# Performance work log

Hardware: AMD Instinct MI355X
Metric: run time of the kernel (lower is better)

The kernel has to match this reference:

```python
import jax, jax.numpy as jnp
import numpy as np

N_QUBITS = 12
N_LAYERS = 2
PATCH = 16
NPS = 14  # patches per side for 224/16
N_PATCHES = NPS * NPS
SCALE = 1.0 / np.sqrt(N_QUBITS)


def _butterfly_gates(n):
    # Faithful replication of QuantumOrthogonalLayer.butterfly_circuit indexing:
    # param_idx increments even when the (idx1, idx2) pair is skipped.
    gates, pidx = [], 0
    n_bl = int(np.ceil(np.log2(n)))
    for layer in range(n_bl):
        stride = 2 ** layer
        for start in range(0, n - stride, 2 * stride):
            for off in range(stride):
                i1, i2 = start + off, start + off + stride
                if i1 < n and i2 < n:
                    gates.append((pidx, i1, i2))
                pidx += 1
    nppl = sum(2 ** (n_bl - 1 - i) * 2 ** i for i in range(n_bl))  # n_params() = 32
    return gates, nppl

GATES, NPPL = _butterfly_gates(N_QUBITS)

# Pauli-Z sign table: qubit 0 is the most-significant bit of the flattened state index.
_bits = (np.arange(2 ** N_QUBITS)[:, None] >> np.arange(N_QUBITS - 1, -1, -1)[None, :]) & 1
Z_SIGNS = jnp.asarray(1.0 - 2.0 * _bits, dtype=jnp.float32)  # (4096, 12)


def _rbs_u(theta):
    # 4x4 real unitary of RY(2t,w1); CNOT(w1,w2); RY(-2t,w1); CNOT(w1,w2)
    c, s = jnp.cos(theta), jnp.sin(theta)
    c2, s2, cs = c * c, s * s, c * s
    return jnp.stack([
        jnp.stack([c2, s2, -cs, cs]),
        jnp.stack([s2, c2, cs, -cs]),
        jnp.stack([cs, -cs, c2, s2]),
        jnp.stack([-cs, cs, s2, c2]),
    ])


def _apply_2q(state, U, i, j):
    # state: (P, 2, 2, ..., 2); apply U to qubit axes i, j
    st = jnp.moveaxis(state, (1 + i, 1 + j), (-2, -1))
    shp = st.shape
    st = st.reshape(shp[:-2] + (4,)) @ U.T
    return jnp.moveaxis(st.reshape(shp), (-2, -1), (1 + i, 1 + j))


@jax.checkpoint
def quantum_expvals(features, params):
    # features: (P, n_qubits) angles; params: (N_LAYERS * NPPL,)
    P = features.shape[0]
    half = 0.5 * features
    amp = jnp.stack([jnp.cos(half), jnp.sin(half)], axis=-1)  # (P, n, 2) RY(x)|0>
    state = jnp.ones((P, 1), features.dtype)
    for q in range(N_QUBITS):  # product-state angle encoding
        state = (state[:, :, None] * amp[:, q][:, None, :]).reshape(P, -1)
    state = state.reshape((P,) + (2,) * N_QUBITS)
    for l in range(N_LAYERS):
        base = l * NPPL
        for pidx, w1, w2 in GATES:
            state = _apply_2q(state, _rbs_u(params[base + pidx]), w1, w2)
    probs = state.reshape(P, -1) ** 2
    return probs @ Z_SIGNS  # (P, n_qubits) <Z_i>


def setup_inputs() -> dict:
    key = jax.random.key(0)
    ks = jax.random.split(key, 6)
    x = jax.random.normal(ks[0], (4, 3, 224, 224), dtype=jnp.float32)
    W_proj = jax.random.normal(ks[1], (N_QUBITS, PATCH * PATCH), dtype=jnp.float32) / np.sqrt(PATCH * PATCH)
    b_proj = jnp.zeros((N_QUBITS,), jnp.float32)
    q_params = 0.1 * jax.random.normal(ks[2], (N_LAYERS * NPPL,), dtype=jnp.float32)
    k_params = 0.1 * jax.random.normal(ks[3], (N_LAYERS * NPPL,), dtype=jnp.float32)
    v_params = 0.1 * jax.random.normal(ks[4], (N_LAYERS * NPPL,), dtype=jnp.float32)
    W_cls = jax.random.normal(ks[5], (1000, N_PATCHES * N_QUBITS), dtype=jnp.float32) / np.sqrt(N_PATCHES * N_QUBITS)
    b_cls = jnp.zeros((1000,), jnp.float32)
    return {"x": x, "W_proj": W_proj, "b_proj": b_proj, "q_params": q_params,
            "k_params": k_params, "v_params": v_params, "W_cls": W_cls, "b_cls": b_cls}


def reference(x, W_proj, b_proj, q_params, k_params, v_params, W_cls, b_cls):
    B = x.shape[0]
    xg = jnp.mean(x, axis=1)  # channel average -> (B, H, W)
    patches = xg.reshape(B, NPS, PATCH, NPS, PATCH).transpose(0, 1, 3, 2, 4)
    patches = patches.reshape(B, N_PATCHES, PATCH * PATCH)
    proj = patches @ W_proj.T + b_proj  # (B, n_patches, n_qubits)
    feats = proj.reshape(-1, N_QUBITS)
    Q = quantum_expvals(feats, q_params).reshape(B, N_PATCHES, N_QUBITS)
    K = quantum_expvals(feats, k_params).reshape(B, N_PATCHES, N_QUBITS)
    V = quantum_expvals(feats, v_params).reshape(B, N_PATCHES, N_QUBITS)
    attn = jax.nn.softmax(jnp.einsum('bqd,bkd->bqk', Q, K) * SCALE, axis=-1)
    out = jnp.einsum('bqk,bkd->bqd', attn, V)  # (B, n_patches, n_qubits)
    logits = out.reshape(B, -1) @ W_cls.T + b_cls
    return logits
```

## Files before the change

kernel.cpp:

```cpp
#include <hip/hip_runtime.h>
#include <math.h>

#define NQ        12
#define NPS       14
#define NPATCH    196
#define NB        4
#define NCLS      1000
#define FEATDIM   2352
#define SCALE_F   0.28867513459481287f

constexpr int PRa[6][5] = {
    { 0, 1, 2, 3, 4},
    { 4, 5, 6, 7, 8},
    { 9,10,11, 0, 8},
    { 0, 4, 5, 8, 1},
    { 1, 6, 9,10, 2},
    { 7,10,11, 2, 3},
};
constexpr int PTa[6][7] = {
    {10, 5, 6, 7,11, 8, 9},
    { 1, 0, 3,10, 2,11, 9},
    { 2, 1, 4, 6, 7, 5, 3},
    { 7, 2, 6, 9,11,10, 3},
    { 0, 7, 4, 5, 8,11, 3},
    { 5, 0, 1, 6, 8, 4, 9},
};
constexpr int  IYa[6]  = {0, 4, 3, 0, 3, 3};
constexpr bool BARa[6] = {false, true, false, false, true, false};

constexpr int cwgt(int X, int q) {
    for (int k = 0; k < 4; ++k) if (PRa[X][k] == q) return 1 << k;
    for (int m = 0; m < 7; ++m) if (PTa[X][m] == q) return 17 << m;
    return 0;
}
constexpr int rimm3(int X, int Y, int IY, int rc) {
    int s = 0;
    for (int j = 0; j < 4; ++j)
        if ((rc >> j) & 1) s += cwgt(X, PRa[Y][j + (j >= IY ? 1 : 0)]);
    return s;
}
constexpr int expand(int rc, int IY) {
    return (rc & ((1 << IY) - 1)) | ((rc >> IY) << (IY + 1));
}

__device__ __forceinline__ void wait_lgkm() {
    __asm__ __volatile__("s_waitcnt lgkmcnt(0)" ::: "memory");
}

template<int TI>
__device__ __forceinline__ void relayout3(float amp[32], float* lds, int tid) {
    constexpr int X = TI, Y = (TI + 1) % 6, IY = IYa[TI];
    constexpr bool BAR = BARa[TI];
    float* w = lds + 17 * tid;
    #pragma unroll
    for (int rc = 0; rc < 16; ++rc) w[rc] = amp[rc];
    if (BAR) __syncthreads(); else wait_lgkm();
    int base = 0;
    #pragma unroll
    for (int j = 0; j < 7; ++j)
        base += ((tid >> j) & 1) ? cwgt(X, PTa[Y][j]) : 0;
    float tmp[16];
    #pragma unroll
    for (int rc = 0; rc < 16; ++rc)
        tmp[rc] = lds[base + rimm3(X, Y, IY, rc)];
    if (BAR) __syncthreads(); else wait_lgkm();
    #pragma unroll
    for (int rc = 0; rc < 16; ++rc) w[rc] = amp[16 + rc];
    if (BAR) __syncthreads(); else wait_lgkm();
    #pragma unroll
    for (int rc = 0; rc < 16; ++rc)
        amp[expand(rc, IY) | (1 << IY)] = lds[base + rimm3(X, Y, IY, rc)];
    if (BAR) __syncthreads();
    #pragma unroll
    for (int rc = 0; rc < 16; ++rc) amp[expand(rc, IY)] = tmp[rc];
}

template<int MI, int MJ>
__device__ __forceinline__ void apply_gate(float amp[32], float gc, float gs) {
    #pragma unroll
    for (int m = 0; m < 32; ++m) {
        if (m & (MI | MJ)) continue;
        float a0 = amp[m], a1 = amp[m | MJ], a2 = amp[m | MI], a3 = amp[m | MI | MJ];
        float p  = a0 + a1, q  = a0 - a1;
        float p2 = a2 + a3, q2 = a2 - a3;
        float t1 = 0.5f * p  + gc * q  - gs * q2;
        float t2 = 0.5f * p2 + gc * q2 + gs * q;
        amp[m]           = t1;
        amp[m | MJ]      = p  - t1;
        amp[m | MI]      = t2;
        amp[m | MI | MJ] = p2 - t2;
    }
}

template<int CTRL>
__device__ __forceinline__ float dppadd(float x) {
    int s = __builtin_amdgcn_update_dpp(0, __float_as_int(x), CTRL, 0xf, 0xf, true);
    return x + __int_as_float(s);
}
__device__ __forceinline__ float wave_sum(float x) {
    x = dppadd<0x111>(x);
    x = dppadd<0x112>(x);
    x = dppadd<0x114>(x);
    x = dppadd<0x118>(x);
    x = dppadd<0x142>(x);
    x = dppadd<0x143>(x);
    return x;
}

__global__ __launch_bounds__(128, 4) void qcirc_kernel(
    const float* __restrict__ x,
    const float* __restrict__ Wp,
    const float* __restrict__ bproj,
    const float* __restrict__ qp,
    const float* __restrict__ kp,
    const float* __restrict__ vp,
    float* __restrict__ qkv)
{
    __shared__ __align__(16) float lds[2176];
    __shared__ float chs[NQ], shs[NQ];
    __shared__ float gC[40], gS[40];
    __shared__ float red2[2][12];

    const int tid = threadIdx.x;
    const int p = blockIdx.x, b = blockIdx.y, c = blockIdx.z;
    const int bp = b * NPATCH + p;
    const float* params = (c == 0) ? qp : (c == 1) ? kp : vp;
    const int lane = tid & 63, wv = tid >> 6;

    float part[NQ];
    #pragma unroll
    for (int q = 0; q < NQ; ++q) part[q] = 0.0f;
    {
        int py = p / NPS, px = p % NPS;
        const float* xb = x + (size_t)b * 3 * 224 * 224;
        #pragma unroll
        for (int k = 0; k < 2; ++k) {
            int pix = tid + 128 * k;
            int off = (py * 16 + (pix >> 4)) * 224 + px * 16 + (pix & 15);
            float v = (xb[off] + xb[off + 50176] + xb[off + 100352]) * (1.0f / 3.0f);
            #pragma unroll
            for (int q = 0; q < NQ; ++q) part[q] += v * Wp[q * 256 + pix];
        }
    }
    if (tid < 40) {
        int l = tid / 20, g = tid - l * 20;
        float th = params[l * 32 + g];
        gC[tid] = 0.5f * cosf(2.0f * th);
        gS[tid] = 0.5f * sinf(2.0f * th);
    }
    #pragma unroll
    for (int q = 0; q < NQ; ++q) part[q] = wave_sum(part[q]);
    if (lane == 63) {
        #pragma unroll
        for (int q = 0; q < NQ; ++q) red2[wv][q] = part[q];
    }
    __syncthreads();
    if (tid < NQ) {
        float h = 0.5f * (red2[0][tid] + red2[1][tid] + bproj[tid]);
        chs[tid] = cosf(h); shs[tid] = sinf(h);
    }
    __syncthreads();

    float amp[32];
    {
        float hi = ((tid &  1) ? shs[10] : chs[10]) *
                   ((tid &  2) ? shs[5]  : chs[5])  *
                   ((tid &  4) ? shs[6]  : chs[6])  *
                   ((tid &  8) ? shs[7]  : chs[7])  *
                   ((tid & 16) ? shs[11] : chs[11]) *
                   ((tid & 32) ? shs[8]  : chs[8])  *
                   ((tid & 64) ? shs[9]  : chs[9]);
        float pA[8], pB[4];
        #pragma unroll
        for (int i = 0; i < 8; ++i)
            pA[i] = ((i & 1) ? shs[0] : chs[0]) * ((i & 2) ? shs[1] : chs[1]) *
                    ((i & 4) ? shs[2] : chs[2]);
        #pragma unroll
        for (int i = 0; i < 4; ++i)
            pB[i] = ((i & 1) ? shs[3] : chs[3]) * ((i & 2) ? shs[4] : chs[4]);
        #pragma unroll
        for (int r = 0; r < 32; ++r) amp[r] = pA[r & 7] * pB[r >> 3] * hi;
    }

    #pragma unroll 1
    for (int l = 0; l < 2; ++l) {
        const int bb = l * 20;
        apply_gate<1, 2>(amp, gC[bb+0], gS[bb+0]);
        apply_gate<4, 8>(amp, gC[bb+1], gS[bb+1]);
        apply_gate<1, 4>(amp, gC[bb+6], gS[bb+6]);
        apply_gate<2, 8>(amp, gC[bb+7], gS[bb+7]);
        relayout3<0>(amp, lds, tid);
        apply_gate<1, 2>(amp, gC[bb+2], gS[bb+2]);
        apply_gate<4, 8>(amp, gC[bb+3], gS[bb+3]);
        apply_gate<1, 4>(amp, gC[bb+8], gS[bb+8]);
        apply_gate<2, 8>(amp, gC[bb+9], gS[bb+9]);
        relayout3<1>(amp, lds, tid);
        apply_gate<16,1>(amp, gC[bb+4],  gS[bb+4]);
        apply_gate<2, 4>(amp, gC[bb+5],  gS[bb+5]);
        apply_gate<16,2>(amp, gC[bb+10], gS[bb+10]);
        apply_gate<1, 4>(amp, gC[bb+11], gS[bb+11]);
        relayout3<2>(amp, lds, tid);
        apply_gate<1, 2>(amp, gC[bb+12], gS[bb+12]);
        apply_gate<16,4>(amp, gC[bb+13], gS[bb+13]);
        apply_gate<1, 8>(amp, gC[bb+16], gS[bb+16]);
        relayout3<3>(amp, lds, tid);
        apply_gate<16,2>(amp, gC[bb+14], gS[bb+14]);
        apply_gate<1, 4>(amp, gC[bb+17], gS[bb+17]);
        relayout3<4>(amp, lds, tid);
        apply_gate<16,1>(amp, gC[bb+15], gS[bb+15]);
        apply_gate<8, 2>(amp, gC[bb+18], gS[bb+18]);
        apply_gate<16,4>(amp, gC[bb+19], gS[bb+19]);
        if (l == 0) relayout3<5>(amp, lds, tid);
    }

    float T, Sq7, Sq10, Sq11, Sq2, Sq3;
    {
        float t1[16]; Sq7 = 0.0f;
        #pragma unroll
        for (int i = 0; i < 16; ++i) {
            float e = amp[2*i] * amp[2*i], o = amp[2*i+1] * amp[2*i+1];
            t1[i] = e + o; Sq7 += e - o;
        }
        float t2[8]; Sq10 = 0.0f;
        #pragma unroll
        for (int i = 0; i < 8; ++i) { t2[i] = t1[2*i] + t1[2*i+1]; Sq10 += t1[2*i] - t1[2*i+1]; }
        float t3[4]; Sq11 = 0.0f;
        #pragma unroll
        for (int i = 0; i < 4; ++i) { t3[i] = t2[2*i] + t2[2*i+1]; Sq11 += t2[2*i] - t2[2*i+1]; }
        float t4[2]; Sq2 = 0.0f;
        #pragma unroll
        for (int i = 0; i < 2; ++i) { t4[i] = t3[2*i] + t3[2*i+1]; Sq2 += t3[2*i] - t3[2*i+1]; }
        T = t4[0] + t4[1]; Sq3 = t4[0] - t4[1];
    }
    float Vq5 = (tid &  1) ? -T : T;
    float Vq0 = (tid &  2) ? -T : T;
    float Vq1 = (tid &  4) ? -T : T;
    float Vq6 = (tid &  8) ? -T : T;
    float Vq8 = (tid & 16) ? -T : T;
    float Vq4 = (tid & 32) ? -T : T;
    T    = wave_sum(T);
    Vq5  = wave_sum(Vq5);  Vq0  = wave_sum(Vq0);  Vq1  = wave_sum(Vq1);
    Vq6  = wave_sum(Vq6);  Vq8  = wave_sum(Vq8);  Vq4  = wave_sum(Vq4);
    Sq7  = wave_sum(Sq7);  Sq10 = wave_sum(Sq10); Sq11 = wave_sum(Sq11);
    Sq2  = wave_sum(Sq2);  Sq3  = wave_sum(Sq3);
    if (lane == 63) {
        red2[wv][0]  = Vq0;  red2[wv][1]  = Vq1;  red2[wv][2]  = Sq2;
        red2[wv][3]  = Sq3;  red2[wv][4]  = Vq4;  red2[wv][5]  = Vq5;
        red2[wv][6]  = Vq6;  red2[wv][7]  = Sq7;  red2[wv][8]  = Vq8;
        red2[wv][9]  = T;    red2[wv][10] = Sq10; red2[wv][11] = Sq11;
    }
    __syncthreads();
    if (tid < NQ) {
        float v1 = red2[1][tid];
        float s = red2[0][tid] + ((tid == 9) ? -v1 : v1);
        qkv[((size_t)c * (NB * NPATCH) + bp) * NQ + tid] = s;
    }
}

__global__ __launch_bounds__(256) void attn_kernel(
    const float* __restrict__ qkv,
    float* __restrict__ outb)
{
    int tid = threadIdx.x;
    int qp = blockIdx.x, b = blockIdx.y;
    const float* Q = qkv;
    const float* K = qkv + NB * NPATCH * NQ;
    const float* V = qkv + 2 * NB * NPATCH * NQ;

    __shared__ float redm[4], reds[4], redv[4][NQ];

    float4 q0 = ((const float4*)(Q + (b * NPATCH + qp) * NQ))[0];
    float4 q1 = ((const float4*)(Q + (b * NPATCH + qp) * NQ))[1];
    float4 q2 = ((const float4*)(Q + (b * NPATCH + qp) * NQ))[2];

    float score = -1e30f;
    float4 v0, v1, v2;
    if (tid < NPATCH) {
        const float4* K4 = (const float4*)(K + (b * NPATCH + tid) * NQ);
        float4 k0 = K4[0], k1 = K4[1], k2 = K4[2];
        float s = q0.x*k0.x + q0.y*k0.y + q0.z*k0.z + q0.w*k0.w
                + q1.x*k1.x + q1.y*k1.y + q1.z*k1.z + q1.w*k1.w
                + q2.x*k2.x + q2.y*k2.y + q2.z*k2.z + q2.w*k2.w;
        score = s * SCALE_F;
        const float4* V4 = (const float4*)(V + (b * NPATCH + tid) * NQ);
        v0 = V4[0]; v1 = V4[1]; v2 = V4[2];
    }
    float m = score;
    #pragma unroll
    for (int o = 32; o > 0; o >>= 1) m = fmaxf(m, __shfl_down(m, o));
    int lane = tid & 63, wv = tid >> 6;
    if (lane == 0) redm[wv] = m;
    __syncthreads();
    float maxv = fmaxf(fmaxf(redm[0], redm[1]), fmaxf(redm[2], redm[3]));

    float w = (tid < NPATCH) ? expf(score - maxv) : 0.0f;
    float sm = w;
    #pragma unroll
    for (int o = 32; o > 0; o >>= 1) sm += __shfl_down(sm, o);
    if (lane == 0) reds[wv] = sm;

    float part[NQ];
    #pragma unroll
    for (int d = 0; d < NQ; d++) part[d] = 0.0f;
    if (tid < NPATCH) {
        part[0] = w*v0.x; part[1] = w*v0.y; part[2]  = w*v0.z; part[3]  = w*v0.w;
        part[4] = w*v1.x; part[5] = w*v1.y; part[6]  = w*v1.z; part[7]  = w*v1.w;
        part[8] = w*v2.x; part[9] = w*v2.y; part[10] = w*v2.z; part[11] = w*v2.w;
    }
    #pragma unroll
    for (int d = 0; d < NQ; d++) {
        #pragma unroll
        for (int o = 32; o > 0; o >>= 1) part[d] += __shfl_down(part[d], o);
    }
    if (lane == 0) {
        #pragma unroll
        for (int d = 0; d < NQ; d++) redv[wv][d] = part[d];
    }
    __syncthreads();
    if (tid < NQ) {
        float sumv = reds[0] + reds[1] + reds[2] + reds[3];
        float s = redv[0][tid] + redv[1][tid] + redv[2][tid] + redv[3][tid];
        outb[(size_t)b * FEATDIM + qp * NQ + tid] = s / sumv;
    }
}

__global__ __launch_bounds__(256) void cls_kernel(
    const float* __restrict__ outb,
    const float* __restrict__ Wc,
    const float* __restrict__ bc,
    float* __restrict__ logits)
{
    int o = blockIdx.x, tid = threadIdx.x;
    float acc[NB] = {0.0f, 0.0f, 0.0f, 0.0f};
    const float4* w4 = (const float4*)(Wc + (size_t)o * FEATDIM);
    for (int j = tid; j < FEATDIM / 4; j += 256) {
        float4 w = w4[j];
        #pragma unroll
        for (int b = 0; b < NB; b++) {
            float4 ov = ((const float4*)(outb + (size_t)b * FEATDIM))[j];
            acc[b] += w.x*ov.x + w.y*ov.y + w.z*ov.z + w.w*ov.w;
        }
    }
    #pragma unroll
    for (int b = 0; b < NB; b++) {
        #pragma unroll
        for (int off = 32; off > 0; off >>= 1) acc[b] += __shfl_down(acc[b], off);
    }
    __shared__ float red[4][NB];
    int lane = tid & 63, wv = tid >> 6;
    if (lane == 0) {
        #pragma unroll
        for (int b = 0; b < NB; b++) red[wv][b] = acc[b];
    }
    __syncthreads();
    if (tid < NB) {
        float s = red[0][tid] + red[1][tid] + red[2][tid] + red[3][tid];
        logits[(size_t)tid * NCLS + o] = s + bc[o];
    }
}

extern "C" void kernel_launch(void* const* d_in, const int* in_sizes, int n_in,
                              void* d_out, int out_size, void* d_ws, size_t ws_size,
                              hipStream_t stream) {
    const float* x     = (const float*)d_in[0];
    const float* Wp    = (const float*)d_in[1];
    const float* bproj = (const float*)d_in[2];
    const float* qp    = (const float*)d_in[3];
    const float* kp    = (const float*)d_in[4];
    const float* vp    = (const float*)d_in[5];
    const float* Wc    = (const float*)d_in[6];
    const float* bc    = (const float*)d_in[7];
    float* logits = (float*)d_out;

    float* ws   = (float*)d_ws;
    float* qkv  = ws;
    float* outb = ws + 28224;

    qcirc_kernel<<<dim3(NPATCH, NB, 3), 128, 0, stream>>>(x, Wp, bproj, qp, kp, vp, qkv);
    attn_kernel <<<dim3(NPATCH, NB),    256, 0, stream>>>(qkv, outb);
    cls_kernel  <<<NCLS,                256, 0, stream>>>(outb, Wc, bc, logits);
}
```

Before: 120.2 us.

## Redesign qubit-to-register mapping with float4 LDS relayouts swapping three qubits

Replaces the six scalar relayout stages, which each exchanged four qubits through LDS in two half passes, with eight relayout stages that keep qubits 2,3 permanently in registers and swap three qubits. Each stage now stores and loads 32 amplitudes as float4 vectors with a 36-float padded stride. The gate schedule, initial product-state ordering and final Pauli-Z reduction are remapped to match. The aim is fewer, wider LDS instructions and fewer waits per relayout, at the cost of more relayout stages and doubling LDS to 4608 floats, which may reduce occupancy.

```diff
diff --git a/kernel.cpp b/kernel.cpp
--- a/kernel.cpp
+++ b/kernel.cpp
@@ -9,38 +9,38 @@
 #define FEATDIM   2352
 #define SCALE_F   0.28867513459481287f
 
-constexpr int PRa[6][5] = {
-    { 0, 1, 2, 3, 4},
-    { 4, 5, 6, 7, 8},
-    { 9,10,11, 0, 8},
-    { 0, 4, 5, 8, 1},
-    { 1, 6, 9,10, 2},
-    { 7,10,11, 2, 3},
+constexpr int PRa[8][5] = {
+    {2,3,0,1, 4},
+    {2,3,4,5, 6},
+    {2,3,5,6, 7},
+    {2,3,0,4, 6},
+    {2,3,8,9,10},
+    {2,3,9,10,11},
+    {2,3,0,8,10},
+    {2,3,1,5, 9},
 };
-constexpr int PTa[6][7] = {
-    {10, 5, 6, 7,11, 8, 9},
-    { 1, 0, 3,10, 2,11, 9},
-    { 2, 1, 4, 6, 7, 5, 3},
-    { 7, 2, 6, 9,11,10, 3},
-    { 0, 7, 4, 5, 8,11, 3},
-    { 5, 0, 1, 6, 8, 4, 9},
+constexpr int PTa[8][7] = {
+    {5,6,7,8,9,10,11},
+    {7,0,1,8,9,10,11},
+    {0,1,4,8,9,10,11},
+    {8,9,10,1,5,7,11},
+    {4,0,1,5,6,7,11},
+    {0,1,8,5,6,7,4},
+    {1,5,9,6,7,11,4},
+    {6,0,11,7,8,10,4},
 };
-constexpr int  IYa[6]  = {0, 4, 3, 0, 3, 3};
-constexpr bool BARa[6] = {false, true, false, false, true, false};
+constexpr bool BARa[8] = {false,false,false,false,true,false,false,true};
 
 constexpr int cwgt(int X, int q) {
-    for (int k = 0; k < 4; ++k) if (PRa[X][k] == q) return 1 << k;
-    for (int m = 0; m < 7; ++m) if (PTa[X][m] == q) return 17 << m;
+    for (int k = 0; k < 5; ++k) if (PRa[X][k] == q) return 1 << k;
+    for (int m = 0; m < 7; ++m) if (PTa[X][m] == q) return 36 << m;
     return 0;
 }
-constexpr int rimm3(int X, int Y, int IY, int rc) {
+constexpr int rimmB(int X, int Y, int a) {
     int s = 0;
-    for (int j = 0; j < 4; ++j)
-        if ((rc >> j) & 1) s += cwgt(X, PRa[Y][j + (j >= IY ? 1 : 0)]);
+    for (int j = 0; j < 3; ++j)
+        if ((a >> j) & 1) s += cwgt(X, PRa[Y][2 + j]);
     return s;
-}
-constexpr int expand(int rc, int IY) {
-    return (rc & ((1 << IY) - 1)) | ((rc >> IY) << (IY + 1));
 }
 
 __device__ __forceinline__ void wait_lgkm() {
@@ -48,31 +48,23 @@
 }
 
 template<int TI>
-__device__ __forceinline__ void relayout3(float amp[32], float* lds, int tid) {
-    constexpr int X = TI, Y = (TI + 1) % 6, IY = IYa[TI];
-    constexpr bool BAR = BARa[TI];
-    float* w = lds + 17 * tid;
-    #pragma unroll
-    for (int rc = 0; rc < 16; ++rc) w[rc] = amp[rc];
-    if (BAR) __syncthreads(); else wait_lgkm();
+__device__ __forceinline__ void relayoutB(float amp[32], float* lds, int tid) {
+    constexpr int X = TI, Y = (TI + 1) & 7;
+    float4* dst = (float4*)(lds + 36 * tid);
+    #pragma unroll
+    for (int k = 0; k < 8; ++k)
+        dst[k] = make_float4(amp[4*k], amp[4*k+1], amp[4*k+2], amp[4*k+3]);
+    if (BARa[TI]) __syncthreads(); else wait_lgkm();
     int base = 0;
     #pragma unroll
     for (int j = 0; j < 7; ++j)
         base += ((tid >> j) & 1) ? cwgt(X, PTa[Y][j]) : 0;
-    float tmp[16];
-    #pragma unroll
-    for (int rc = 0; rc < 16; ++rc)
-        tmp[rc] = lds[base + rimm3(X, Y, IY, rc)];
-    if (BAR) __syncthreads(); else wait_lgkm();
-    #pragma unroll
-    for (int rc = 0; rc < 16; ++rc) w[rc] = amp[16 + rc];
-    if (BAR) __syncthreads(); else wait_lgkm();
-    #pragma unroll
-    for (int rc = 0; rc < 16; ++rc)
-        amp[expand(rc, IY) | (1 << IY)] = lds[base + rimm3(X, Y, IY, rc)];
-    if (BAR) __syncthreads();
-    #pragma unroll
-    for (int rc = 0; rc < 16; ++rc) amp[expand(rc, IY)] = tmp[rc];
+    #pragma unroll
+    for (int a = 0; a < 8; ++a) {
+        float4 v = *(const float4*)(lds + base + rimmB(X, Y, a));
+        amp[4*a+0] = v.x; amp[4*a+1] = v.y; amp[4*a+2] = v.z; amp[4*a+3] = v.w;
+    }
+    if (BARa[TI]) __syncthreads();
 }
 
 template<int MI, int MJ>
@@ -116,7 +108,7 @@
     const float* __restrict__ vp,
     float* __restrict__ qkv)
 {
-    __shared__ __align__(16) float lds[2176];
+    __shared__ __align__(16) float lds[4608];
     __shared__ float chs[NQ], shs[NQ];
     __shared__ float gC[40], gS[40];
     __shared__ float red2[2][12];
@@ -163,21 +155,21 @@
 
     float amp[32];
     {
-        float hi = ((tid &  1) ? shs[10] : chs[10]) *
-                   ((tid &  2) ? shs[5]  : chs[5])  *
-                   ((tid &  4) ? shs[6]  : chs[6])  *
-                   ((tid &  8) ? shs[7]  : chs[7])  *
-                   ((tid & 16) ? shs[11] : chs[11]) *
-                   ((tid & 32) ? shs[8]  : chs[8])  *
-                   ((tid & 64) ? shs[9]  : chs[9]);
+        float hi = ((tid &  1) ? shs[5]  : chs[5])  *
+                   ((tid &  2) ? shs[6]  : chs[6])  *
+                   ((tid &  4) ? shs[7]  : chs[7])  *
+                   ((tid &  8) ? shs[8]  : chs[8])  *
+                   ((tid & 16) ? shs[9]  : chs[9])  *
+                   ((tid & 32) ? shs[10] : chs[10]) *
+                   ((tid & 64) ? shs[11] : chs[11]);
         float pA[8], pB[4];
         #pragma unroll
         for (int i = 0; i < 8; ++i)
-            pA[i] = ((i & 1) ? shs[0] : chs[0]) * ((i & 2) ? shs[1] : chs[1]) *
-                    ((i & 4) ? shs[2] : chs[2]);
+            pA[i] = ((i & 1) ? shs[2] : chs[2]) * ((i & 2) ? shs[3] : chs[3]) *
+                    ((i & 4) ? shs[0] : chs[0]);
         #pragma unroll
         for (int i = 0; i < 4; ++i)
-            pB[i] = ((i & 1) ? shs[3] : chs[3]) * ((i & 2) ? shs[4] : chs[4]);
+            pB[i] = ((i & 1) ? shs[1] : chs[1]) * ((i & 2) ? shs[4] : chs[4]);
         #pragma unroll
         for (int r = 0; r < 32; ++r) amp[r] = pA[r & 7] * pB[r >> 3] * hi;
     }
@@ -185,74 +177,76 @@
     #pragma unroll 1
     for (int l = 0; l < 2; ++l) {
         const int bb = l * 20;
-        apply_gate<1, 2>(amp, gC[bb+0], gS[bb+0]);
-        apply_gate<4, 8>(amp, gC[bb+1], gS[bb+1]);
-        apply_gate<1, 4>(amp, gC[bb+6], gS[bb+6]);
-        apply_gate<2, 8>(amp, gC[bb+7], gS[bb+7]);
-        relayout3<0>(amp, lds, tid);
-        apply_gate<1, 2>(amp, gC[bb+2], gS[bb+2]);
-        apply_gate<4, 8>(amp, gC[bb+3], gS[bb+3]);
-        apply_gate<1, 4>(amp, gC[bb+8], gS[bb+8]);
-        apply_gate<2, 8>(amp, gC[bb+9], gS[bb+9]);
-        relayout3<1>(amp, lds, tid);
-        apply_gate<16,1>(amp, gC[bb+4],  gS[bb+4]);
-        apply_gate<2, 4>(amp, gC[bb+5],  gS[bb+5]);
-        apply_gate<16,2>(amp, gC[bb+10], gS[bb+10]);
-        apply_gate<1, 4>(amp, gC[bb+11], gS[bb+11]);
-        relayout3<2>(amp, lds, tid);
-        apply_gate<1, 2>(amp, gC[bb+12], gS[bb+12]);
-        apply_gate<16,4>(amp, gC[bb+13], gS[bb+13]);
-        apply_gate<1, 8>(amp, gC[bb+16], gS[bb+16]);
-        relayout3<3>(amp, lds, tid);
-        apply_gate<16,2>(amp, gC[bb+14], gS[bb+14]);
-        apply_gate<1, 4>(amp, gC[bb+17], gS[bb+17]);
-        relayout3<4>(amp, lds, tid);
-        apply_gate<16,1>(amp, gC[bb+15], gS[bb+15]);
-        apply_gate<8, 2>(amp, gC[bb+18], gS[bb+18]);
-        apply_gate<16,4>(amp, gC[bb+19], gS[bb+19]);
-        if (l == 0) relayout3<5>(amp, lds, tid);
-    }
-
-    float T, Sq7, Sq10, Sq11, Sq2, Sq3;
+        apply_gate<4, 8>(amp, gC[bb+0], gS[bb+0]);
+        apply_gate<1, 2>(amp, gC[bb+1], gS[bb+1]);
+        apply_gate<4, 1>(amp, gC[bb+6], gS[bb+6]);
+        apply_gate<8, 2>(amp, gC[bb+7], gS[bb+7]);
+        relayoutB<0>(amp, lds, tid);
+        apply_gate<4, 8>(amp, gC[bb+2], gS[bb+2]);
+        relayoutB<1>(amp, lds, tid);
+        apply_gate<8,16>(amp, gC[bb+3],  gS[bb+3]);
+        apply_gate<4,16>(amp, gC[bb+9],  gS[bb+9]);
+        apply_gate<2,16>(amp, gC[bb+15], gS[bb+15]);
+        relayoutB<2>(amp, lds, tid);
+        apply_gate<8,16>(amp, gC[bb+8],  gS[bb+8]);
+        apply_gate<4, 8>(amp, gC[bb+12], gS[bb+12]);
+        apply_gate<1,16>(amp, gC[bb+14], gS[bb+14]);
+        relayoutB<3>(amp, lds, tid);
+        apply_gate<4, 8>(amp, gC[bb+4], gS[bb+4]);
+        relayoutB<4>(amp, lds, tid);
+        apply_gate<8,16>(amp, gC[bb+5],  gS[bb+5]);
+        apply_gate<4,16>(amp, gC[bb+11], gS[bb+11]);
+        apply_gate<2,16>(amp, gC[bb+19], gS[bb+19]);
+        relayoutB<5>(amp, lds, tid);
+        apply_gate<8,16>(amp, gC[bb+10], gS[bb+10]);
+        apply_gate<4, 8>(amp, gC[bb+16], gS[bb+16]);
+        apply_gate<1,16>(amp, gC[bb+18], gS[bb+18]);
+        relayoutB<6>(amp, lds, tid);
+        apply_gate<4, 8>(amp, gC[bb+13], gS[bb+13]);
+        apply_gate<4,16>(amp, gC[bb+17], gS[bb+17]);
+        if (l == 0) relayoutB<7>(amp, lds, tid);
+    }
+
+    float T, Sq2, Sq3, Sq1, Sq5, Sq9;
     {
-        float t1[16]; Sq7 = 0.0f;
+        float t1[16]; Sq2 = 0.0f;
         #pragma unroll
         for (int i = 0; i < 16; ++i) {
             float e = amp[2*i] * amp[2*i], o = amp[2*i+1] * amp[2*i+1];
-            t1[i] = e + o; Sq7 += e - o;
+            t1[i] = e + o; Sq2 += e - o;
         }
-        float t2[8]; Sq10 = 0.0f;
-        #pragma unroll
-        for (int i = 0; i < 8; ++i) { t2[i] = t1[2*i] + t1[2*i+1]; Sq10 += t1[2*i] - t1[2*i+1]; }
-        float t3[4]; Sq11 = 0.0f;
-        #pragma unroll
-        for (int i = 0; i < 4; ++i) { t3[i] = t2[2*i] + t2[2*i+1]; Sq11 += t2[2*i] - t2[2*i+1]; }
-        float t4[2]; Sq2 = 0.0f;
-        #pragma unroll
-        for (int i = 0; i < 2; ++i) { t4[i] = t3[2*i] + t3[2*i+1]; Sq2 += t3[2*i] - t3[2*i+1]; }
-        T = t4[0] + t4[1]; Sq3 = t4[0] - t4[1];
-    }
-    float Vq5 = (tid &  1) ? -T : T;
-    float Vq0 = (tid &  2) ? -T : T;
-    float Vq1 = (tid &  4) ? -T : T;
-    float Vq6 = (tid &  8) ? -T : T;
-    float Vq8 = (tid & 16) ? -T : T;
-    float Vq4 = (tid & 32) ? -T : T;
+        float t2[8]; Sq3 = 0.0f;
+        #pragma unroll
+        for (int i = 0; i < 8; ++i) { t2[i] = t1[2*i] + t1[2*i+1]; Sq3 += t1[2*i] - t1[2*i+1]; }
+        float t3[4]; Sq1 = 0.0f;
+        #pragma unroll
+        for (int i = 0; i < 4; ++i) { t3[i] = t2[2*i] + t2[2*i+1]; Sq1 += t2[2*i] - t2[2*i+1]; }
+        float t4[2]; Sq5 = 0.0f;
+        #pragma unroll
+        for (int i = 0; i < 2; ++i) { t4[i] = t3[2*i] + t3[2*i+1]; Sq5 += t3[2*i] - t3[2*i+1]; }
+        T = t4[0] + t4[1]; Sq9 = t4[0] - t4[1];
+    }
+    float Vq6  = (tid &  1) ? -T : T;
+    float Vq0  = (tid &  2) ? -T : T;
+    float Vq11 = (tid &  4) ? -T : T;
+    float Vq7  = (tid &  8) ? -T : T;
+    float Vq8  = (tid & 16) ? -T : T;
+    float Vq10 = (tid & 32) ? -T : T;
     T    = wave_sum(T);
-    Vq5  = wave_sum(Vq5);  Vq0  = wave_sum(Vq0);  Vq1  = wave_sum(Vq1);
-    Vq6  = wave_sum(Vq6);  Vq8  = wave_sum(Vq8);  Vq4  = wave_sum(Vq4);
-    Sq7  = wave_sum(Sq7);  Sq10 = wave_sum(Sq10); Sq11 = wave_sum(Sq11);
-    Sq2  = wave_sum(Sq2);  Sq3  = wave_sum(Sq3);
+    Vq6  = wave_sum(Vq6);  Vq0  = wave_sum(Vq0);  Vq11 = wave_sum(Vq11);
+    Vq7  = wave_sum(Vq7);  Vq8  = wave_sum(Vq8);  Vq10 = wave_sum(Vq10);
+    Sq2  = wave_sum(Sq2);  Sq3  = wave_sum(Sq3);  Sq1  = wave_sum(Sq1);
+    Sq5  = wave_sum(Sq5);  Sq9  = wave_sum(Sq9);
     if (lane == 63) {
-        red2[wv][0]  = Vq0;  red2[wv][1]  = Vq1;  red2[wv][2]  = Sq2;
-        red2[wv][3]  = Sq3;  red2[wv][4]  = Vq4;  red2[wv][5]  = Vq5;
-        red2[wv][6]  = Vq6;  red2[wv][7]  = Sq7;  red2[wv][8]  = Vq8;
-        red2[wv][9]  = T;    red2[wv][10] = Sq10; red2[wv][11] = Sq11;
+        red2[wv][0]  = Vq0;  red2[wv][1]  = Sq1;  red2[wv][2]  = Sq2;
+        red2[wv][3]  = Sq3;  red2[wv][4]  = T;    red2[wv][5]  = Sq5;
+        red2[wv][6]  = Vq6;  red2[wv][7]  = Vq7;  red2[wv][8]  = Vq8;
+        red2[wv][9]  = Sq9;  red2[wv][10] = Vq10; red2[wv][11] = Vq11;
     }
     __syncthreads();
     if (tid < NQ) {
         float v1 = red2[1][tid];
-        float s = red2[0][tid] + ((tid == 9) ? -v1 : v1);
+        float s = red2[0][tid] + ((tid == 4) ? -v1 : v1);
         qkv[((size_t)c * (NB * NPATCH) + bp) * NQ + tid] = s;
     }
 }
```

After: 122.1 us. Within noise of the previous version (+1.6%).
